# Kernel tuning notes

Measured on AMD Instinct MI355X. Metric: run time of the kernel, lower is better.

## Reference

```python
import jax, jax.numpy as jnp
import numpy as np

HIDDEN = 768
HEADS = 12
HEAD_DIM = HIDDEN // HEADS


def setup_inputs() -> dict:
    key = jax.random.key(0)
    ks = jax.random.split(key, 5)
    B, S = 1, 4096
    scale = 1.0 / np.sqrt(HIDDEN)
    return {
        "x": jax.random.normal(ks[0], (B, S, HIDDEN), dtype=jnp.float32),
        "w_qkv": jax.random.normal(ks[1], (HIDDEN, 3 * HIDDEN), dtype=jnp.float32) * scale,
        "b_qkv": jnp.zeros((3 * HIDDEN,), dtype=jnp.float32),
        "w_proj": jax.random.normal(ks[2], (HIDDEN, HIDDEN), dtype=jnp.float32) * scale,
        "b_proj": jnp.zeros((HIDDEN,), dtype=jnp.float32),
    }


def reference(x, w_qkv, b_qkv, w_proj, b_proj):
    B, S, D = x.shape
    H, Hd = HEADS, HEAD_DIM
    qkv = x @ w_qkv + b_qkv                        # [B,S,3D]
    qkv = qkv.reshape(B, S, 3, H, Hd)
    q, k, v = (jnp.moveaxis(qkv[:, :, i], 2, 1) for i in range(3))  # [B,H,S,Hd]
    scale = 1.0 / np.sqrt(Hd)
    attn = jnp.einsum("bhqd,bhkd->bhqk", q, k) * scale
    attn = jax.nn.softmax(attn, axis=-1)
    o = jnp.einsum("bhqk,bhkd->bhqd", attn, v)     # [B,H,S,Hd]
    o = jnp.moveaxis(o, 1, 2).reshape(B, S, D)
    return o @ w_proj + b_proj
```

## Files before the change

### kernel.cpp

```cpp
#include <hip/hip_runtime.h>

#define S_LEN 4096
#define DMODEL 768
#define NHEAD 12
#define HDIM 64
#define DQKV 2304

typedef __attribute__((ext_vector_type(8))) __bf16 bf16x8;
typedef __attribute__((ext_vector_type(4))) float f32x4;
typedef __attribute__((ext_vector_type(8))) unsigned short ushort8;

#define LOG2E 1.4426950408889634f

#if __has_builtin(__builtin_amdgcn_exp2f)
#define EXP2(x) __builtin_amdgcn_exp2f(x)
#else
#define EXP2(x) exp2f(x)
#endif

static __device__ __forceinline__ unsigned short f2bf(float f) {
  unsigned int u = __float_as_uint(f);
  u += 0x7FFFu + ((u >> 16) & 1u);
  return (unsigned short)(u >> 16);
}

static __device__ __forceinline__ void gload_lds16(const unsigned short* g, unsigned short* l) {
  __builtin_amdgcn_global_load_lds(
      (const __attribute__((address_space(1))) unsigned int*)g,
      (__attribute__((address_space(3))) unsigned int*)l, 16, 0, 0);
}

__global__ __launch_bounds__(256) void k_convert(const float* __restrict__ in,
                                                 unsigned short* __restrict__ out,
                                                 int n) {
  int i = (blockIdx.x * 256 + threadIdx.x) * 8;
  if (i >= n) return;
  const float4* p = reinterpret_cast<const float4*>(in + i);
  float4 a = p[0], b = p[1];
  ushort8 r;
  r[0] = f2bf(a.x); r[1] = f2bf(a.y); r[2] = f2bf(a.z); r[3] = f2bf(a.w);
  r[4] = f2bf(b.x); r[5] = f2bf(b.y); r[6] = f2bf(b.z); r[7] = f2bf(b.w);
  *reinterpret_cast<ushort8*>(out + i) = r;
}

__global__ __launch_bounds__(256) void k_transpose(const float* __restrict__ in,
                                                   unsigned short* __restrict__ out,
                                                   int Kdim, int Ndim) {
  __shared__ unsigned short t[64 * 65];
  int k0 = blockIdx.y * 64, n0 = blockIdx.x * 64;
  int tid = threadIdx.x;
#pragma unroll
  for (int p = 0; p < 4; ++p) {
    int r = p * 16 + (tid >> 4);
    int c = (tid & 15) * 4;
    float4 v = *reinterpret_cast<const float4*>(in + (size_t)(k0 + r) * Ndim + n0 + c);
    t[(c + 0) * 65 + r] = f2bf(v.x);
    t[(c + 1) * 65 + r] = f2bf(v.y);
    t[(c + 2) * 65 + r] = f2bf(v.z);
    t[(c + 3) * 65 + r] = f2bf(v.w);
  }
  __syncthreads();
#pragma unroll
  for (int p = 0; p < 2; ++p) {
    int task = p * 256 + tid;
    int rr = task >> 3;
    int cc = (task & 7) * 8;
    ushort8 r;
#pragma unroll
    for (int j = 0; j < 8; ++j) r[j] = t[rr * 65 + cc + j];
    *reinterpret_cast<ushort8*>(out + (size_t)(n0 + rr) * Kdim + k0 + cc) = r;
  }
}

template <int MODE>
__global__ __launch_bounds__(256) void k_gemm(const unsigned short* __restrict__ A,
                                              const unsigned short* __restrict__ Bt,
                                              const float* __restrict__ bias,
                                              unsigned short* __restrict__ Qb,
                                              unsigned short* __restrict__ Kf,
                                              unsigned short* __restrict__ Vf,
                                              float* __restrict__ outf) {
  __shared__ unsigned short As[2][128 * 32];
  __shared__ unsigned short Bs[2][128 * 32];

  int tid = threadIdx.x;
  int lane = tid & 63, wave = tid >> 6;
  int wr = wave >> 1, wc = wave & 1;
  int m0 = blockIdx.y * 128, n0 = blockIdx.x * 128;
  int r16 = lane & 15, g = lane >> 4;

  int ca0 = wave * 2, ca1 = wave * 2 + 1;
  int srow = lane >> 2, scol = (lane & 3) * 8;

  f32x4 acc[4][4] = {};

#define GSTAGE(BUF, K0)                                                                 \
  do {                                                                                  \
    gload_lds16(A + (size_t)(m0 + ca0 * 16 + srow) * DMODEL + (K0) + scol,              \
                &As[BUF][ca0 * 512]);                                                   \
    gload_lds16(A + (size_t)(m0 + ca1 * 16 + srow) * DMODEL + (K0) + scol,              \
                &As[BUF][ca1 * 512]);                                                   \
    gload_lds16(Bt + (size_t)(n0 + ca0 * 16 + srow) * DMODEL + (K0) + scol,             \
                &Bs[BUF][ca0 * 512]);                                                   \
    gload_lds16(Bt + (size_t)(n0 + ca1 * 16 + srow) * DMODEL + (K0) + scol,             \
                &Bs[BUF][ca1 * 512]);                                                   \
  } while (0)

  GSTAGE(0, 0);
  for (int kt = 0; kt < DMODEL / 32; ++kt) {
    int cur = kt & 1;
    __syncthreads();

    bf16x8 af[4], bfr[4];
#pragma unroll
    for (int m = 0; m < 4; ++m)
      af[m] = *reinterpret_cast<const bf16x8*>(&As[cur][(wr * 64 + m * 16 + r16) * 32 + g * 8]);
#pragma unroll
    for (int n = 0; n < 4; ++n)
      bfr[n] = *reinterpret_cast<const bf16x8*>(&Bs[cur][(wc * 64 + n * 16 + r16) * 32 + g * 8]);

    if (kt < DMODEL / 32 - 1) GSTAGE(cur ^ 1, (kt + 1) * 32);

#pragma unroll
    for (int m = 0; m < 4; ++m)
#pragma unroll
      for (int n = 0; n < 4; ++n)
        acc[m][n] = __builtin_amdgcn_mfma_f32_16x16x32_bf16(af[m], bfr[n], acc[m][n], 0, 0, 0);
  }
#undef GSTAGE

#pragma unroll
  for (int m = 0; m < 4; ++m) {
    int grow0 = m0 + wr * 64 + m * 16 + 4 * g;
#pragma unroll
    for (int n = 0; n < 4; ++n) {
      int gcol = n0 + wc * 64 + n * 16 + r16;
      float bv = bias[gcol];
      if (MODE == 0) {
        int sect = gcol / DMODEL;
        int rem = gcol - sect * DMODEL;
        int h = rem >> 6, hd = rem & 63;
        if (sect == 2) {
          int j = hd >> 4, r16v = hd & 15;
          int tile = grow0 >> 6, kk = (grow0 >> 5) & 1, g2 = (grow0 >> 3) & 3, e0 = grow0 & 7;
          size_t base = (((size_t)h * 64 + tile) * 8 + (j * 2 + kk)) * 512 +
                        (size_t)(g2 * 16 + r16v) * 8 + e0;
          ushort4 pk;
          pk.x = f2bf(acc[m][n][0] + bv);
          pk.y = f2bf(acc[m][n][1] + bv);
          pk.z = f2bf(acc[m][n][2] + bv);
          pk.w = f2bf(acc[m][n][3] + bv);
          *reinterpret_cast<ushort4*>(Vf + base) = pk;
        } else if (sect == 0) {
#pragma unroll
          for (int i = 0; i < 4; ++i)
            Qb[((size_t)h * S_LEN + grow0 + i) * HDIM + hd] =
                f2bf((acc[m][n][i] + bv) * (0.125f * LOG2E));
        } else {
          int kk = hd >> 5, g2 = (hd >> 3) & 3, e = hd & 7;
#pragma unroll
          for (int i = 0; i < 4; ++i) {
            int s = grow0 + i;
            int tile = s >> 6, r = s & 63;
            int j = (((r >> 2) & 1) << 1) | (r >> 5);
            int r16l = (r & 3) | (((r >> 3) & 3) << 2);
            size_t idx = (((size_t)h * 64 + tile) * 8 + (j * 2 + kk)) * 512 +
                         (size_t)(g2 * 16 + r16l) * 8 + e;
            Kf[idx] = f2bf(acc[m][n][i] + bv);
          }
        }
      } else {
#pragma unroll
        for (int i = 0; i < 4; ++i)
          outf[(size_t)(grow0 + i) * DMODEL + gcol] = acc[m][n][i] + bv;
      }
    }
  }
}

__global__ __launch_bounds__(256, 3) void k_attn(const unsigned short* __restrict__ Q,
                                                 const unsigned short* __restrict__ Kf,
                                                 const unsigned short* __restrict__ Vf,
                                                 unsigned short* __restrict__ O) {
  __shared__ unsigned short ldsK[2][4096];
  __shared__ unsigned short ldsV[2][4096];

  int tid = threadIdx.x;
  int lane = tid & 63, wave = tid >> 6;
  int r16 = lane & 15, g = lane >> 4;

  int bid = blockIdx.x;
  int gid = (bid & 7) * 96 + (bid >> 3);
  int h = gid >> 6;
  int qbase = (gid & 63) * 64 + wave * 16;

  const unsigned short* KfH = Kf + (size_t)h * (64 * 4096);
  const unsigned short* VfH = Vf + (size_t)h * (64 * 4096);

  const unsigned short* qptr = Q + ((size_t)h * S_LEN + qbase + r16) * HDIM + g * 8;
  bf16x8 qf0 = *reinterpret_cast<const bf16x8*>(qptr);
  bf16x8 qf1 = *reinterpret_cast<const bf16x8*>(qptr + 32);

  f32x4 oacc[4] = {};
  f32x4 lsum = {};
  f32x4 zinit = {};
  float mrow = 0.f;
  bf16x8 bones;
#pragma unroll
  for (int e = 0; e < 8; ++e) bones[e] = (__bf16)1.0f;

  int c0 = wave, c1 = wave + 4;

#define STAGE(BUF, T)                                                        \
  do {                                                                       \
    const unsigned short* kg_ = KfH + (size_t)(T) * 4096;                    \
    const unsigned short* vg_ = VfH + (size_t)(T) * 4096;                    \
    gload_lds16(kg_ + c0 * 512 + lane * 8, &ldsK[BUF][c0 * 512]);            \
    gload_lds16(kg_ + c1 * 512 + lane * 8, &ldsK[BUF][c1 * 512]);            \
    gload_lds16(vg_ + c0 * 512 + lane * 8, &ldsV[BUF][c0 * 512]);            \
    gload_lds16(vg_ + c1 * 512 + lane * 8, &ldsV[BUF][c1 * 512]);            \
  } while (0)

#define TILE_COMPUTE(KFR, VFR, FIRST)                                                   \
  do {                                                                                  \
    f32x4 s_[4];                                                                        \
    _Pragma("unroll") for (int j_ = 0; j_ < 4; ++j_) {                                  \
      f32x4 z_ = zinit;                                                                 \
      z_ = __builtin_amdgcn_mfma_f32_16x16x32_bf16(KFR[2 * j_], qf0, z_, 0, 0, 0);      \
      s_[j_] = __builtin_amdgcn_mfma_f32_16x16x32_bf16(KFR[2 * j_ + 1], qf1, z_, 0, 0, 0); \
    }                                                                                   \
                               \
    float x1_ = fmaxf(fmaxf(s_[0][0], s_[0][1]), s_[0][2]);                             \
    float x2_ = fmaxf(fmaxf(s_[0][3], s_[1][0]), s_[1][1]);                             \
    float x3_ = fmaxf(fmaxf(s_[1][2], s_[1][3]), s_[2][0]);                             \
    float x4_ = fmaxf(fmaxf(s_[2][1], s_[2][2]), s_[2][3]);                             \
    float x5_ = fmaxf(fmaxf(s_[3][0], s_[3][1]), s_[3][2]);                             \
    float pm_ = fmaxf(fmaxf(fmaxf(x1_, x2_), fmaxf(x3_, x4_)), fmaxf(x5_, s_[3][3]));   \
    pm_ = fmaxf(pm_, __shfl_xor(pm_, 16));                                              \
    pm_ = fmaxf(pm_, __shfl_xor(pm_, 32));                                              \
    if (FIRST) {                                                                        \
                              \
      _Pragma("unroll") for (int j_ = 0; j_ < 4; ++j_)                                  \
        _Pragma("unroll") for (int i_ = 0; i_ < 4; ++i_) s_[j_][i_] -= pm_;             \
      mrow = pm_;                                                                       \
      zinit[0] = -mrow; zinit[1] = -mrow; zinit[2] = -mrow; zinit[3] = -mrow;           \
    } else if (__any(pm_ > 8.f)) {             \
      float dl_ = fmaxf(pm_, 0.f);                                                      \
      float al_ = EXP2(-dl_);                                                           \
      float a0_ = __shfl(al_, 20 * g + 0), a1_ = __shfl(al_, 20 * g + 1);               \
      float a2_ = __shfl(al_, 20 * g + 2), a3_ = __shfl(al_, 20 * g + 3);               \
      lsum[0] *= a0_; lsum[1] *= a1_; lsum[2] *= a2_; lsum[3] *= a3_;                   \
      _Pragma("unroll") for (int j_ = 0; j_ < 4; ++j_) {                                \
        oacc[j_][0] *= a0_; oacc[j_][1] *= a1_;                                         \
        oacc[j_][2] *= a2_; oacc[j_][3] *= a3_;                                         \
      }                                                                                 \
      _Pragma("unroll") for (int j_ = 0; j_ < 4; ++j_)                                  \
        _Pragma("unroll") for (int i_ = 0; i_ < 4; ++i_) s_[j_][i_] -= dl_;             \
      mrow += dl_;                                                                      \
      zinit[0] = -mrow; zinit[1] = -mrow; zinit[2] = -mrow; zinit[3] = -mrow;           \
    }                                                                                   \
    float p_[4][4];                                                                     \
    _Pragma("unroll") for (int j_ = 0; j_ < 4; ++j_)                                    \
      _Pragma("unroll") for (int i_ = 0; i_ < 4; ++i_)                                  \
        p_[j_][i_] = EXP2(s_[j_][i_]);                                                  \
                            \
    bf16x8 pa0_, pa1_;                                                                  \
    _Pragma("unroll") for (int e_ = 0; e_ < 8; ++e_) {                                  \
      pa0_[e_] = (__bf16)p_[2 * (e_ >> 2)][e_ & 3];                                     \
      pa1_[e_] = (__bf16)p_[1 + 2 * (e_ >> 2)][e_ & 3];                                 \
    }                                                                                   \
                         \
    lsum = __builtin_amdgcn_mfma_f32_16x16x32_bf16(pa0_, bones, lsum, 0, 0, 0);         \
    lsum = __builtin_amdgcn_mfma_f32_16x16x32_bf16(pa1_, bones, lsum, 0, 0, 0);         \
    _Pragma("unroll") for (int j_ = 0; j_ < 4; ++j_) {                                  \
      oacc[j_] = __builtin_amdgcn_mfma_f32_16x16x32_bf16(pa0_, VFR[2 * j_], oacc[j_], 0, 0, 0); \
      oacc[j_] = __builtin_amdgcn_mfma_f32_16x16x32_bf16(pa1_, VFR[2 * j_ + 1], oacc[j_], 0, 0, 0); \
    }                                                                                   \
  } while (0)

#define BODY(T, CUR, DO_STAGE, FIRSTF)                                                  \
  do {                                                                                  \
    __syncthreads();          \
    bf16x8 kfr_[8], vfr_[8];                                                            \
    _Pragma("unroll") for (int f_ = 0; f_ < 8; ++f_) {                                  \
      kfr_[f_] = *reinterpret_cast<const bf16x8*>(&ldsK[CUR][f_ * 512 + lane * 8]);     \
      vfr_[f_] = *reinterpret_cast<const bf16x8*>(&ldsV[CUR][f_ * 512 + lane * 8]);     \
    }                                                                                   \
    if (DO_STAGE) STAGE((CUR) ^ 1, (T) + 1);                                            \
    TILE_COMPUTE(kfr_, vfr_, FIRSTF);                                                   \
  } while (0)

  STAGE(0, 0);
  BODY(0, 0, true, true);
  for (int pr = 0; pr < 31; ++pr) {
    BODY(2 * pr + 1, 1, true, false);
    BODY(2 * pr + 2, 0, true, false);
  }
  BODY(63, 1, false, false);
#undef BODY
#undef TILE_COMPUTE
#undef STAGE

#pragma unroll
  for (int i = 0; i < 4; ++i) {
    float linv = 1.0f / lsum[i];
    int srow = qbase + 4 * g + i;
#pragma unroll
    for (int j = 0; j < 4; ++j) {
      int col = h * HDIM + j * 16 + r16;
      O[(size_t)srow * DMODEL + col] = f2bf(oacc[j][i] * linv);
    }
  }
}

extern "C" void kernel_launch(void* const* d_in, const int* in_sizes, int n_in,
                              void* d_out, int out_size, void* d_ws, size_t ws_size,
                              hipStream_t stream) {
  const float* x = (const float*)d_in[0];
  const float* w_qkv = (const float*)d_in[1];
  const float* b_qkv = (const float*)d_in[2];
  const float* w_proj = (const float*)d_in[3];
  const float* b_proj = (const float*)d_in[4];
  float* out = (float*)d_out;

  unsigned short* ws16 = (unsigned short*)d_ws;
  unsigned short* xb = ws16;
  unsigned short* wqkvT = xb + (size_t)S_LEN * DMODEL;
  unsigned short* wprojT = wqkvT + (size_t)DQKV * DMODEL;
  unsigned short* Qb = wprojT + (size_t)DMODEL * DMODEL;
  unsigned short* Kf = Qb + (size_t)NHEAD * S_LEN * HDIM;
  unsigned short* Vf = Kf + (size_t)NHEAD * S_LEN * HDIM;
  unsigned short* Ob = xb;

  k_convert<<<(S_LEN * DMODEL) / (256 * 8), 256, 0, stream>>>(x, xb, S_LEN * DMODEL);
  k_transpose<<<dim3(DQKV / 64, DMODEL / 64), 256, 0, stream>>>(w_qkv, wqkvT, DMODEL, DQKV);
  k_transpose<<<dim3(DMODEL / 64, DMODEL / 64), 256, 0, stream>>>(w_proj, wprojT, DMODEL, DMODEL);
  k_gemm<0><<<dim3(DQKV / 128, S_LEN / 128), 256, 0, stream>>>(xb, wqkvT, b_qkv, Qb, Kf, Vf, nullptr);
  k_attn<<<768, 256, 0, stream>>>(Qb, Kf, Vf, Ob);
  k_gemm<1><<<dim3(DMODEL / 128, S_LEN / 128), 256, 0, stream>>>(Ob, wprojT, b_proj, nullptr, nullptr, nullptr, out);
}
```

Baseline: 135.6 us.

## Load K/V fragments directly from global memory instead of LDS double buffering

The attention kernel drops its shared-memory double buffer for K and V tiles, along with the per-tile barrier. Each wave now reads its MFMA fragments straight from global memory, which is already laid out in fragment order. This removes the barrier and LDS traffic and frees LDS for occupancy. In exchange, all four waves in a block load the same K/V data separately, relying on L1/L2 hits, and the loads no longer overlap with compute through explicit prefetching.

```diff
diff --git a/kernel.cpp b/kernel.cpp
--- a/kernel.cpp
+++ b/kernel.cpp
@@ -182,9 +182,6 @@
                                                  const unsigned short* __restrict__ Kf,
                                                  const unsigned short* __restrict__ Vf,
                                                  unsigned short* __restrict__ O) {
-  __shared__ unsigned short ldsK[2][4096];
-  __shared__ unsigned short ldsV[2][4096];
-
   int tid = threadIdx.x;
   int lane = tid & 63, wave = tid >> 6;
   int r16 = lane & 15, g = lane >> 4;
@@ -194,8 +191,9 @@
   int h = gid >> 6;
   int qbase = (gid & 63) * 64 + wave * 16;
 
-  const unsigned short* KfH = Kf + (size_t)h * (64 * 4096);
-  const unsigned short* VfH = Vf + (size_t)h * (64 * 4096);
+  const unsigned short* kb = Kf + (size_t)h * (64 * 4096);
+  const unsigned short* vb = Vf + (size_t)h * (64 * 4096);
+  int loff = lane * 8;
 
   const unsigned short* qptr = Q + ((size_t)h * S_LEN + qbase + r16) * HDIM + g * 8;
   bf16x8 qf0 = *reinterpret_cast<const bf16x8*>(qptr);
@@ -208,18 +206,6 @@
   bf16x8 bones;
 #pragma unroll
   for (int e = 0; e < 8; ++e) bones[e] = (__bf16)1.0f;
-
-  int c0 = wave, c1 = wave + 4;
-
-#define STAGE(BUF, T)                                                        \
-  do {                                                                       \
-    const unsigned short* kg_ = KfH + (size_t)(T) * 4096;                    \
-    const unsigned short* vg_ = VfH + (size_t)(T) * 4096;                    \
-    gload_lds16(kg_ + c0 * 512 + lane * 8, &ldsK[BUF][c0 * 512]);            \
-    gload_lds16(kg_ + c1 * 512 + lane * 8, &ldsK[BUF][c1 * 512]);            \
-    gload_lds16(vg_ + c0 * 512 + lane * 8, &ldsV[BUF][c0 * 512]);            \
-    gload_lds16(vg_ + c1 * 512 + lane * 8, &ldsV[BUF][c1 * 512]);            \
-  } while (0)
 
 #define TILE_COMPUTE(KFR, VFR, FIRST)                                                   \
   do {                                                                                  \
@@ -278,28 +264,25 @@
     }                                                                                   \
   } while (0)
 
-#define BODY(T, CUR, DO_STAGE, FIRSTF)                                                  \
+#define BODY(FIRSTF)                                                                    \
   do {                                                                                  \
-    __syncthreads();          \
     bf16x8 kfr_[8], vfr_[8];                                                            \
-    _Pragma("unroll") for (int f_ = 0; f_ < 8; ++f_) {                                  \
-      kfr_[f_] = *reinterpret_cast<const bf16x8*>(&ldsK[CUR][f_ * 512 + lane * 8]);     \
-      vfr_[f_] = *reinterpret_cast<const bf16x8*>(&ldsV[CUR][f_ * 512 + lane * 8]);     \
-    }                                                                                   \
-    if (DO_STAGE) STAGE((CUR) ^ 1, (T) + 1);                                            \
+    _Pragma("unroll") for (int f_ = 0; f_ < 8; ++f_)                                    \
+      kfr_[f_] = *reinterpret_cast<const bf16x8*>(kb + f_ * 512 + loff);                \
+    _Pragma("unroll") for (int f_ = 0; f_ < 8; ++f_)                                    \
+      vfr_[f_] = *reinterpret_cast<const bf16x8*>(vb + f_ * 512 + loff);                \
     TILE_COMPUTE(kfr_, vfr_, FIRSTF);                                                   \
+    kb += 4096;                                                                         \
+    vb += 4096;                                                                         \
   } while (0)
 
-  STAGE(0, 0);
-  BODY(0, 0, true, true);
-  for (int pr = 0; pr < 31; ++pr) {
-    BODY(2 * pr + 1, 1, true, false);
-    BODY(2 * pr + 2, 0, true, false);
-  }
-  BODY(63, 1, false, false);
+  BODY(true);
+#pragma unroll 2
+  for (int t = 1; t < 64; ++t) {
+    BODY(false);
+  }
 #undef BODY
 #undef TILE_COMPUTE
-#undef STAGE
 
 #pragma unroll
   for (int i = 0; i < 4; ++i) {
```

New measurement: 159.2 us. 17.4% more time.

## Process two query sub-tiles per wave in attention to reuse K/V fragments

Applied to the files above, without the earlier changes.

The attention kernel drops from four waves per block, each owning 16 query rows, to two waves per block, each owning 32 query rows as two independent 16-row sub-tiles. The K/V fragments read from LDS are shared by both sub-tiles, which halves LDS read traffic per query row and gives the scheduler two independent softmax/MFMA chains to interleave. Each wave now stages four K and four V chunks instead of two of each. The cost is higher register pressure and half as many waves per CU for the same 768-block grid, so there is less latency hiding from occupancy.

```diff
diff --git a/kernel.cpp b/kernel.cpp
--- a/kernel.cpp
+++ b/kernel.cpp
@@ -178,7 +178,7 @@
   }
 }
 
-__global__ __launch_bounds__(256, 3) void k_attn(const unsigned short* __restrict__ Q,
+__global__ __launch_bounds__(128, 2) void k_attn(const unsigned short* __restrict__ Q,
                                                  const unsigned short* __restrict__ Kf,
                                                  const unsigned short* __restrict__ Vf,
                                                  unsigned short* __restrict__ O) {
@@ -192,24 +192,28 @@
   int bid = blockIdx.x;
   int gid = (bid & 7) * 96 + (bid >> 3);
   int h = gid >> 6;
-  int qbase = (gid & 63) * 64 + wave * 16;
+  int qbaseA = (gid & 63) * 64 + wave * 16;
+  int qbaseB = qbaseA + 32;
 
   const unsigned short* KfH = Kf + (size_t)h * (64 * 4096);
   const unsigned short* VfH = Vf + (size_t)h * (64 * 4096);
 
-  const unsigned short* qptr = Q + ((size_t)h * S_LEN + qbase + r16) * HDIM + g * 8;
-  bf16x8 qf0 = *reinterpret_cast<const bf16x8*>(qptr);
-  bf16x8 qf1 = *reinterpret_cast<const bf16x8*>(qptr + 32);
-
-  f32x4 oacc[4] = {};
-  f32x4 lsum = {};
-  f32x4 zinit = {};
-  float mrow = 0.f;
+  const unsigned short* qpA = Q + ((size_t)h * S_LEN + qbaseA + r16) * HDIM + g * 8;
+  const unsigned short* qpB = Q + ((size_t)h * S_LEN + qbaseB + r16) * HDIM + g * 8;
+  bf16x8 qf0a = *reinterpret_cast<const bf16x8*>(qpA);
+  bf16x8 qf1a = *reinterpret_cast<const bf16x8*>(qpA + 32);
+  bf16x8 qf0b = *reinterpret_cast<const bf16x8*>(qpB);
+  bf16x8 qf1b = *reinterpret_cast<const bf16x8*>(qpB + 32);
+
+  f32x4 oaccA[4] = {}, oaccB[4] = {};
+  f32x4 lsumA = {}, lsumB = {};
+  f32x4 zinitA = {}, zinitB = {};
+  float mrowA = 0.f, mrowB = 0.f;
   bf16x8 bones;
 #pragma unroll
   for (int e = 0; e < 8; ++e) bones[e] = (__bf16)1.0f;
 
-  int c0 = wave, c1 = wave + 4;
+  int c0 = wave * 4, c1 = c0 + 1, c2 = c0 + 2, c3 = c0 + 3;
 
 #define STAGE(BUF, T)                                                        \
   do {                                                                       \
@@ -217,68 +221,71 @@
     const unsigned short* vg_ = VfH + (size_t)(T) * 4096;                    \
     gload_lds16(kg_ + c0 * 512 + lane * 8, &ldsK[BUF][c0 * 512]);            \
     gload_lds16(kg_ + c1 * 512 + lane * 8, &ldsK[BUF][c1 * 512]);            \
+    gload_lds16(kg_ + c2 * 512 + lane * 8, &ldsK[BUF][c2 * 512]);            \
+    gload_lds16(kg_ + c3 * 512 + lane * 8, &ldsK[BUF][c3 * 512]);            \
     gload_lds16(vg_ + c0 * 512 + lane * 8, &ldsV[BUF][c0 * 512]);            \
     gload_lds16(vg_ + c1 * 512 + lane * 8, &ldsV[BUF][c1 * 512]);            \
-  } while (0)
-
-#define TILE_COMPUTE(KFR, VFR, FIRST)                                                   \
+    gload_lds16(vg_ + c2 * 512 + lane * 8, &ldsV[BUF][c2 * 512]);            \
+    gload_lds16(vg_ + c3 * 512 + lane * 8, &ldsV[BUF][c3 * 512]);            \
+  } while (0)
+
+#define QK(SARR, QF0, QF1, ZI)                                                          \
   do {                                                                                  \
-    f32x4 s_[4];                                                                        \
     _Pragma("unroll") for (int j_ = 0; j_ < 4; ++j_) {                                  \
-      f32x4 z_ = zinit;                                                                 \
-      z_ = __builtin_amdgcn_mfma_f32_16x16x32_bf16(KFR[2 * j_], qf0, z_, 0, 0, 0);      \
-      s_[j_] = __builtin_amdgcn_mfma_f32_16x16x32_bf16(KFR[2 * j_ + 1], qf1, z_, 0, 0, 0); \
-    }                                                                                   \
-                               \
-    float x1_ = fmaxf(fmaxf(s_[0][0], s_[0][1]), s_[0][2]);                             \
-    float x2_ = fmaxf(fmaxf(s_[0][3], s_[1][0]), s_[1][1]);                             \
-    float x3_ = fmaxf(fmaxf(s_[1][2], s_[1][3]), s_[2][0]);                             \
-    float x4_ = fmaxf(fmaxf(s_[2][1], s_[2][2]), s_[2][3]);                             \
-    float x5_ = fmaxf(fmaxf(s_[3][0], s_[3][1]), s_[3][2]);                             \
-    float pm_ = fmaxf(fmaxf(fmaxf(x1_, x2_), fmaxf(x3_, x4_)), fmaxf(x5_, s_[3][3]));   \
+      f32x4 z_ = ZI;                                                                    \
+      z_ = __builtin_amdgcn_mfma_f32_16x16x32_bf16(kfr_[2 * j_], QF0, z_, 0, 0, 0);     \
+      SARR[j_] = __builtin_amdgcn_mfma_f32_16x16x32_bf16(kfr_[2 * j_ + 1], QF1, z_, 0, 0, 0); \
+    }                                                                                   \
+  } while (0)
+
+#define SOFTPV(SARR, MROW, ZI, LSUM, OACC, FIRST)                                       \
+  do {                                                                                  \
+    float x1_ = fmaxf(fmaxf(SARR[0][0], SARR[0][1]), SARR[0][2]);                       \
+    float x2_ = fmaxf(fmaxf(SARR[0][3], SARR[1][0]), SARR[1][1]);                       \
+    float x3_ = fmaxf(fmaxf(SARR[1][2], SARR[1][3]), SARR[2][0]);                       \
+    float x4_ = fmaxf(fmaxf(SARR[2][1], SARR[2][2]), SARR[2][3]);                       \
+    float x5_ = fmaxf(fmaxf(SARR[3][0], SARR[3][1]), SARR[3][2]);                       \
+    float pm_ = fmaxf(fmaxf(fmaxf(x1_, x2_), fmaxf(x3_, x4_)), fmaxf(x5_, SARR[3][3])); \
     pm_ = fmaxf(pm_, __shfl_xor(pm_, 16));                                              \
     pm_ = fmaxf(pm_, __shfl_xor(pm_, 32));                                              \
     if (FIRST) {                                                                        \
-                              \
       _Pragma("unroll") for (int j_ = 0; j_ < 4; ++j_)                                  \
-        _Pragma("unroll") for (int i_ = 0; i_ < 4; ++i_) s_[j_][i_] -= pm_;             \
-      mrow = pm_;                                                                       \
-      zinit[0] = -mrow; zinit[1] = -mrow; zinit[2] = -mrow; zinit[3] = -mrow;           \
-    } else if (__any(pm_ > 8.f)) {             \
+        _Pragma("unroll") for (int i_ = 0; i_ < 4; ++i_) SARR[j_][i_] -= pm_;           \
+      MROW = pm_;                                                                       \
+      ZI[0] = -MROW; ZI[1] = -MROW; ZI[2] = -MROW; ZI[3] = -MROW;                       \
+    } else if (__any(pm_ > 8.f)) {                                                      \
       float dl_ = fmaxf(pm_, 0.f);                                                      \
       float al_ = EXP2(-dl_);                                                           \
       float a0_ = __shfl(al_, 20 * g + 0), a1_ = __shfl(al_, 20 * g + 1);               \
       float a2_ = __shfl(al_, 20 * g + 2), a3_ = __shfl(al_, 20 * g + 3);               \
-      lsum[0] *= a0_; lsum[1] *= a1_; lsum[2] *= a2_; lsum[3] *= a3_;                   \
+      LSUM[0] *= a0_; LSUM[1] *= a1_; LSUM[2] *= a2_; LSUM[3] *= a3_;                   \
       _Pragma("unroll") for (int j_ = 0; j_ < 4; ++j_) {                                \
-        oacc[j_][0] *= a0_; oacc[j_][1] *= a1_;                                         \
-        oacc[j_][2] *= a2_; oacc[j_][3] *= a3_;                                         \
+        OACC[j_][0] *= a0_; OACC[j_][1] *= a1_;                                         \
+        OACC[j_][2] *= a2_; OACC[j_][3] *= a3_;                                         \
       }                                                                                 \
       _Pragma("unroll") for (int j_ = 0; j_ < 4; ++j_)                                  \
-        _Pragma("unroll") for (int i_ = 0; i_ < 4; ++i_) s_[j_][i_] -= dl_;             \
-      mrow += dl_;                                                                      \
-      zinit[0] = -mrow; zinit[1] = -mrow; zinit[2] = -mrow; zinit[3] = -mrow;           \
+        _Pragma("unroll") for (int i_ = 0; i_ < 4; ++i_) SARR[j_][i_] -= dl_;           \
+      MROW += dl_;                                                                      \
+      ZI[0] = -MROW; ZI[1] = -MROW; ZI[2] = -MROW; ZI[3] = -MROW;                       \
     }                                                                                   \
     float p_[4][4];                                                                     \
     _Pragma("unroll") for (int j_ = 0; j_ < 4; ++j_)                                    \
       _Pragma("unroll") for (int i_ = 0; i_ < 4; ++i_)                                  \
-        p_[j_][i_] = EXP2(s_[j_][i_]);                                                  \
-                            \
+        p_[j_][i_] = EXP2(SARR[j_][i_]);                                                \
     bf16x8 pa0_, pa1_;                                                                  \
     _Pragma("unroll") for (int e_ = 0; e_ < 8; ++e_) {                                  \
       pa0_[e_] = (__bf16)p_[2 * (e_ >> 2)][e_ & 3];                                     \
       pa1_[e_] = (__bf16)p_[1 + 2 * (e_ >> 2)][e_ & 3];                                 \
     }                                                                                   \
-                         \
-    lsum = __builtin_amdgcn_mfma_f32_16x16x32_bf16(pa0_, bones, lsum, 0, 0, 0);         \
-    lsum = __builtin_amdgcn_mfma_f32_16x16x32_bf16(pa1_, bones, lsum, 0, 0, 0);         \
+    LSUM = __builtin_amdgcn_mfma_f32_16x16x32_bf16(pa0_, bones, LSUM, 0, 0, 0);         \
+    LSUM = __builtin_amdgcn_mfma_f32_16x16x32_bf16(pa1_, bones, LSUM, 0, 0, 0);         \
     _Pragma("unroll") for (int j_ = 0; j_ < 4; ++j_) {                                  \
-      oacc[j_] = __builtin_amdgcn_mfma_f32_16x16x32_bf16(pa0_, VFR[2 * j_], oacc[j_], 0, 0, 0); \
-      oacc[j_] = __builtin_amdgcn_mfma_f32_16x16x32_bf16(pa1_, VFR[2 * j_ + 1], oacc[j_], 0, 0, 0); \
-    }                                                                                   \
-  } while (0)
-
-#define BODY(T, CUR, DO_STAGE, FIRSTF)                                                  \
+      OACC[j_] = __builtin_amdgcn_mfma_f32_16x16x32_bf16(pa0_, vfr_[2 * j_], OACC[j_], 0, 0, 0); \
+      OACC[j_] = __builtin_amdgcn_mfma_f32_16x16x32_bf16(pa1_, vfr_[2 * j_ + 1], OACC[j_], 0, 0, 0); \
+    }                                                                                   \
+  } while (0)
+
+#define BODY(CUR, DO_STAGE, T, FIRSTF)                                                  \
   do {                                                                                  \
     __syncthreads();          \
     bf16x8 kfr_[8], vfr_[8];                                                            \
@@ -287,28 +294,36 @@
       vfr_[f_] = *reinterpret_cast<const bf16x8*>(&ldsV[CUR][f_ * 512 + lane * 8]);     \
     }                                                                                   \
     if (DO_STAGE) STAGE((CUR) ^ 1, (T) + 1);                                            \
-    TILE_COMPUTE(kfr_, vfr_, FIRSTF);                                                   \
+    f32x4 sA_[4], sB_[4];                                                               \
+    QK(sA_, qf0a, qf1a, zinitA);                                                        \
+    QK(sB_, qf0b, qf1b, zinitB);                                                        \
+    SOFTPV(sA_, mrowA, zinitA, lsumA, oaccA, FIRSTF);                                   \
+    SOFTPV(sB_, mrowB, zinitB, lsumB, oaccB, FIRSTF);                                   \
   } while (0)
 
   STAGE(0, 0);
-  BODY(0, 0, true, true);
+  BODY(0, true, 0, true);
   for (int pr = 0; pr < 31; ++pr) {
-    BODY(2 * pr + 1, 1, true, false);
-    BODY(2 * pr + 2, 0, true, false);
-  }
-  BODY(63, 1, false, false);
+    BODY(1, true, 2 * pr + 1, false);
+    BODY(0, true, 2 * pr + 2, false);
+  }
+  BODY(1, false, 63, false);
 #undef BODY
-#undef TILE_COMPUTE
+#undef SOFTPV
+#undef QK
 #undef STAGE
 
 #pragma unroll
   for (int i = 0; i < 4; ++i) {
-    float linv = 1.0f / lsum[i];
-    int srow = qbase + 4 * g + i;
+    float linvA = 1.0f / lsumA[i];
+    float linvB = 1.0f / lsumB[i];
+    int srowA = qbaseA + 4 * g + i;
+    int srowB = qbaseB + 4 * g + i;
 #pragma unroll
     for (int j = 0; j < 4; ++j) {
       int col = h * HDIM + j * 16 + r16;
-      O[(size_t)srow * DMODEL + col] = f2bf(oacc[j][i] * linv);
+      O[(size_t)srowA * DMODEL + col] = f2bf(oaccA[j][i] * linvA);
+      O[(size_t)srowB * DMODEL + col] = f2bf(oaccB[j][i] * linvB);
     }
   }
 }
@@ -336,6 +351,6 @@
   k_transpose<<<dim3(DQKV / 64, DMODEL / 64), 256, 0, stream>>>(w_qkv, wqkvT, DMODEL, DQKV);
   k_transpose<<<dim3(DMODEL / 64, DMODEL / 64), 256, 0, stream>>>(w_proj, wprojT, DMODEL, DMODEL);
   k_gemm<0><<<dim3(DQKV / 128, S_LEN / 128), 256, 0, stream>>>(xb, wqkvT, b_qkv, Qb, Kf, Vf, nullptr);
-  k_attn<<<768, 256, 0, stream>>>(Qb, Kf, Vf, Ob);
+  k_attn<<<768, 128, 0, stream>>>(Qb, Kf, Vf, Ob);
   k_gemm<1><<<dim3(DMODEL / 128, S_LEN / 128), 256, 0, stream>>>(Ob, wprojT, b_proj, nullptr, nullptr, nullptr, out);
 }
```

New measurement: 139.4 us. 2.8% more time.
